# Kernel tuning notes

Hardware: AMD Instinct MI355X
Metric: run time of the kernel (lower is better)

Reference implementation:

```python
import jax, jax.numpy as jnp
import numpy as np

N_QUBITS = 12
N_LAYERS = 6
BATCH = 8192
D_IN = 512


def _apply_1q(state, gate, wire):
    # state: [B] + [2]*n (real), gate: [2,2]. new[j] = sum_i gate[j,i]*old[i]
    s = jnp.moveaxis(state, 1 + wire, -1)
    s = jnp.einsum('...i,ji->...j', s, gate)
    return jnp.moveaxis(s, -1, 1 + wire)


def _apply_cnot(state, ctrl, tgt):
    # flip target amplitude pair where control bit == 1
    s = jnp.moveaxis(state, (1 + ctrl, 1 + tgt), (-2, -1))
    s = jnp.concatenate([s[..., :1, :], s[..., 1:, ::-1]], axis=-2)
    return jnp.moveaxis(s, (-2, -1), (1 + ctrl, 1 + tgt))


def _simulate(angles, weights):
    # angles: [B, n] per-sample RY angles; weights: [L, n] shared RY angles.
    # Circuit: H + RY(angle) per wire on |0>, then L x (RY layer + CNOT chain).
    # All gates are real -> real float32 statevector.
    B, n = angles.shape
    L = weights.shape[0]
    inv_sqrt2 = jnp.float32(1.0 / np.sqrt(2.0))
    half = 0.5 * angles
    c, s = jnp.cos(half), jnp.sin(half)
    # per-wire single-qubit state RY(a) @ H @ |0> = inv_sqrt2 * [c-s, c+s]
    v = inv_sqrt2 * jnp.stack([c - s, c + s], axis=-1)  # [B, n, 2]
    state = v[:, 0]  # [B, 2]
    for w in range(1, n):
        state = jnp.einsum('b...,bj->b...j', state, v[:, w])  # product state
    # state: [B] + [2]*n
    for layer in range(L):
        h = 0.5 * weights[layer]
        cl, sl = jnp.cos(h), jnp.sin(h)
        for w in range(n):
            gate = jnp.stack([jnp.stack([cl[w], -sl[w]]),
                              jnp.stack([sl[w], cl[w]])])
            state = _apply_1q(state, gate, w)
        for w in range(n - 1):
            state = _apply_cnot(state, w, w + 1)
    probs = state * state
    zs = []
    for w in range(n):
        axes = tuple(a for a in range(1, n + 1) if a != 1 + w)
        p = probs.sum(axis=axes)  # [B, 2]
        zs.append(p[:, 0] - p[:, 1])
    return jnp.stack(zs, axis=-1)  # [B, n] = <Z_i>


def setup_inputs() -> dict:
    key = jax.random.key(0)
    ks = jax.random.split(key, 6)
    x = jax.random.normal(ks[0], (BATCH, D_IN), jnp.float32)
    pre_w = jax.random.normal(ks[1], (N_QUBITS, D_IN), jnp.float32) / np.sqrt(D_IN)
    pre_b = jax.random.normal(ks[2], (N_QUBITS,), jnp.float32) * 0.01
    weights = jax.random.normal(ks[3], (N_LAYERS, N_QUBITS), jnp.float32)
    post_w = jax.random.normal(ks[4], (1, N_QUBITS), jnp.float32) / np.sqrt(N_QUBITS)
    post_b = jax.random.normal(ks[5], (1,), jnp.float32) * 0.01
    return {"x": x, "pre_w": pre_w, "pre_b": pre_b, "weights": weights,
            "post_w": post_w, "post_b": post_b}


def reference(x, pre_w, pre_b, weights, post_w, post_b):
    pre = x @ pre_w.T + pre_b                # [B, n_qubits]
    angles = pre * jnp.float32(np.pi / 2.0)  # RY(inputs[i]*pi/2)
    q_out = _simulate(angles, weights)       # [B, n_qubits]
    return q_out @ post_w.T + post_b         # [B, 1]
```

## Files before the change

### kernel.cpp

```cpp
#include <hip/hip_runtime.h>
#include <math.h>

#define NQ 12
#define NL 6
#define BATCHN 8192
#define DIN 512

typedef _Float16 f16;
typedef __attribute__((ext_vector_type(8)))  _Float16 f16x8;
typedef __attribute__((ext_vector_type(16))) float    f32x16;
typedef unsigned int u32;
typedef __attribute__((ext_vector_type(4))) u32 u32x4;
typedef __attribute__((ext_vector_type(2))) int i32x2;


__device__ __forceinline__ u32 pkrtz(float a, float b) {
  auto p = __builtin_amdgcn_cvt_pkrtz(a, b);
  return __builtin_bit_cast(u32, p);
}
__device__ __forceinline__ u32 bperm(int addr, u32 v) {
  return (u32)__builtin_amdgcn_ds_bpermute(addr, (int)v);
}
__device__ __forceinline__ float dppx1(float v) {
  return __int_as_float(__builtin_amdgcn_mov_dpp(__float_as_int(v), 0xB1, 0xF, 0xF, true));
}
__device__ __forceinline__ u32 dppx1u(u32 v) {
  return (u32)__builtin_amdgcn_mov_dpp((int)v, 0xB1, 0xF, 0xF, true);
}
__device__ __forceinline__ float dppx2(float v) {
  return __int_as_float(__builtin_amdgcn_mov_dpp(__float_as_int(v), 0x4E, 0xF, 0xF, true));
}
__device__ __forceinline__ float dppx8(float v) {
  return __int_as_float(__builtin_amdgcn_mov_dpp(__float_as_int(v), 0x128, 0xF, 0xF, true));
}
template <int PAT>
__device__ __forceinline__ float swzf(float v) {
  return __int_as_float(__builtin_amdgcn_ds_swizzle(__float_as_int(v), PAT));
}

#if __has_builtin(__builtin_amdgcn_permlane32_swap)
__device__ __forceinline__ void pswap(u32& a, u32& b) {
  i32x2 r = __builtin_amdgcn_permlane32_swap((int)a, (int)b, false, false);
  a = (u32)r.x; b = (u32)r.y;
}
#else
#define PSWAP_FALLBACK 1
__device__ __forceinline__ void pswap_fb(u32& a, u32& b, bool hi, int axor) {
  u32 xa = bperm(axor, a), xb = bperm(axor, b);
  u32 na = hi ? xb : a;
  u32 nb = hi ? b : xa;
  a = na; b = nb;
}
#endif

__device__ __forceinline__ float wave_sum(float v) {
  v += dppx1(v);
  v += dppx2(v);
  v += swzf<0x101F>(v);
  v += dppx8(v);
  v += swzf<0x401F>(v);
#ifndef PSWAP_FALLBACK
  u32 a = __builtin_bit_cast(u32, v), b = a;
  pswap(a, b);
  return __builtin_bit_cast(float, a) + __builtin_bit_cast(float, b);
#else
  return v + __shfl_xor(v, 32, 64);
#endif
}
__device__ __forceinline__ f16x8 asf(const u32 a[4]) {
  u32x4 v; v.x = a[0]; v.y = a[1]; v.z = a[2]; v.w = a[3];
  return __builtin_bit_cast(f16x8, v);
}
__device__ __forceinline__ f16x8 ldB(const u32* __restrict__ p, int off) {
  u32x4 v = *(const u32x4*)(p + off);
  return __builtin_bit_cast(f16x8, v);
}

__device__ __forceinline__ void sincos_rev(float rev, float* s, float* c) {
  float r = rev - floorf(rev);
#if __has_builtin(__builtin_amdgcn_sinf) && __has_builtin(__builtin_amdgcn_cosf)
  *s = __builtin_amdgcn_sinf(r);
  *c = __builtin_amdgcn_cosf(r);
#else
  const float TWO_PI = 6.28318530717958647693f;
  sincosf(r * TWO_PI, s, c);
#endif
}

__device__ __forceinline__ u32 foldw(u32 w, u32 m) {
  u32 partner = dppx1u(w);
  return (m & partner) | (~m & w);
}

__global__ void setup_mats(const float* __restrict__ weights, u32* __restrict__ Bbuf) {
  const int mm = blockIdx.x >> 3;
  const int l  = mm >> 1;
  const int qs = mm & 1;
  __shared__ float c6[6], s6[6];
  if (threadIdx.x < 6) {
    float h = 0.5f * weights[l * NQ + qs * 6 + threadIdx.x];
    c6[threadIdx.x] = cosf(h);
    s6[threadIdx.x] = sinf(h);
  }
  __syncthreads();
  const int t = (blockIdx.x & 7) * 256 + threadIdx.x;
  const int lane = (t >> 2) & 63;
  const int fk   = t >> 8;
  const int kt   = fk & 3;
  const int nt   = fk >> 2;
  const int n     = nt * 32 + (lane & 31);
  const int kbase = kt * 16 + (lane >> 5) * 8 + (t & 3) * 2;
  float v[2];
  #pragma unroll
  for (int u = 0; u < 2; ++u) {
    int k = kbase + u;
    int bb = k;
    if (l >= 1) { bb ^= bb << 1; bb ^= bb << 2; bb ^= bb << 4; bb &= 63; }
    float prod = 1.f;
    #pragma unroll
    for (int w = 0; w < 6; ++w) {
      const int aw = (n >> w) & 1, bw = (bb >> w) & 1;
      prod *= (aw == bw) ? c6[w] : (aw ? s6[w] : -s6[w]);
    }
    v[u] = prod;
  }
  Bbuf[mm * 2048 + t] = pkrtz(v[0], v[1]);
}

template <bool FOLD>
__device__ __forceinline__ void mm_step(f32x16 (&d)[2][2],
                                        const u32* __restrict__ Bl,
                                        u32 maskA, u32 maskB) {
  f16x8 Bc0 = ldB(Bl, 0 * 256);
  f16x8 Bc1 = ldB(Bl, 4 * 256);
  u32 fr[2][4][4];
  #pragma unroll
  for (int kt = 0; kt < 4; ++kt) {
    const int s  = kt >> 1;
    const int b0 = 4 * ((2 * kt) & 3);
    const int b1 = 4 * ((2 * kt + 1) & 3);
    #pragma unroll
    for (int mt = 0; mt < 2; ++mt) {
      u32 p0a = pkrtz(d[s][mt][b0 + 0], d[s][mt][b0 + 1]);
      u32 p0b = pkrtz(d[s][mt][b0 + 2], d[s][mt][b0 + 3]);
      u32 p1a = pkrtz(d[s][mt][b1 + 0], d[s][mt][b1 + 1]);
      u32 p1b = pkrtz(d[s][mt][b1 + 2], d[s][mt][b1 + 3]);
      if (FOLD) {
        const int PAR4[4] = {0, 1, 1, 0};
        const int ka = (PAR4[b0 >> 2] + s) & 1;
        const int kc = (PAR4[b1 >> 2] + s) & 1;
        p0a = foldw(p0a, ka ? maskB : maskA);
        p0b = foldw(p0b, ka ? maskA : maskB);
        p1a = foldw(p1a, kc ? maskB : maskA);
        p1b = foldw(p1b, kc ? maskA : maskB);
      }
#ifdef PSWAP_FALLBACK
      pswap_fb(p0a, p1a, false, 0);
      pswap_fb(p0b, p1b, false, 0);
#else
      pswap(p0a, p1a);
      pswap(p0b, p1b);
#endif
      fr[mt][kt][0] = p0a;
      fr[mt][kt][1] = p0b;
      fr[mt][kt][2] = p1a;
      fr[mt][kt][3] = p1b;
    }
  }
  #pragma unroll
  for (int kt = 0; kt < 4; ++kt) {
    f16x8 B0 = Bc0, B1 = Bc1;
    if (kt < 3) {
      Bc0 = ldB(Bl, (kt + 1) * 256);
      Bc1 = ldB(Bl, (4 + kt + 1) * 256);
    }
    f16x8 A0 = asf(fr[0][kt]);
    f16x8 A1 = asf(fr[1][kt]);
    if (kt == 0) {
      f32x16 z{};
      d[0][0] = __builtin_amdgcn_mfma_f32_32x32x16_f16(A0, B0, z, 0, 0, 0);
      d[0][1] = __builtin_amdgcn_mfma_f32_32x32x16_f16(A0, B1, z, 0, 0, 0);
      d[1][0] = __builtin_amdgcn_mfma_f32_32x32x16_f16(A1, B0, z, 0, 0, 0);
      d[1][1] = __builtin_amdgcn_mfma_f32_32x32x16_f16(A1, B1, z, 0, 0, 0);
    } else {
      d[0][0] = __builtin_amdgcn_mfma_f32_32x32x16_f16(A0, B0, d[0][0], 0, 0, 0);
      d[0][1] = __builtin_amdgcn_mfma_f32_32x32x16_f16(A0, B1, d[0][1], 0, 0, 0);
      d[1][0] = __builtin_amdgcn_mfma_f32_32x32x16_f16(A1, B0, d[1][0], 0, 0, 0);
      d[1][1] = __builtin_amdgcn_mfma_f32_32x32x16_f16(A1, B1, d[1][1], 0, 0, 0);
    }
  }
}

__global__ void __launch_bounds__(256) __attribute__((amdgpu_waves_per_eu(4, 8)))
dqc_main(const float* __restrict__ x,
         const float* __restrict__ pre_w,
         const float* __restrict__ pre_b,
         const float* __restrict__ weights,
         const float* __restrict__ post_w,
         const float* __restrict__ post_b,
         const u32* __restrict__ Bbuf,
         float* __restrict__ out)
{
  const int lane = threadIdx.x & 63;
  const bool hi  = lane >= 32;
  const int b    = blockIdx.x * 4 + (threadIdx.x >> 6);
  const u32 maskA = hi ? 0x0000FFFFu : 0xFFFF0000u;
  const u32 maskB = ~maskA;

  float acc[NQ];
  const float* xr = x + (size_t)b * DIN + lane * 8;
  const float4 xa = *(const float4*)(xr);
  const float4 xb = *(const float4*)(xr + 4);
  #pragma unroll
  for (int w = 0; w < NQ; ++w) {
    const float* wr = pre_w + w * DIN + lane * 8;
    const float4 wa = *(const float4*)(wr);
    const float4 wb = *(const float4*)(wr + 4);
    acc[w] = xa.x * wa.x + xa.y * wa.y + xa.z * wa.z + xa.w * wa.w
           + xb.x * wb.x + xb.y * wb.y + xb.z * wb.z + xb.w * wb.w;
  }
  #pragma unroll
  for (int w = 0; w < NQ; ++w) acc[w] = wave_sum(acc[w]);

  const float INV_4PI = 0.07957747154594766788f;
  float u0[NQ], u1[NQ];
  #pragma unroll
  for (int w = 0; w < NQ; ++w) {
    const float cw2 = 0.125f + pre_b[w] * 0.125f + weights[w] * INV_4PI;
    const float rev = fmaf(acc[w], 0.125f, cw2);
    sincos_rev(rev, &u1[w], &u0[w]);
  }

  float base8[8];
  #pragma unroll
  for (int j = 0; j < 8; ++j)
    base8[j] = ((j & 1) ? u1[0] : u0[0]) * ((j & 2) ? u1[1] : u0[1]) * ((j & 4) ? u1[2] : u0[2]);
  float hiP[4];
  #pragma unroll
  for (int kt = 0; kt < 4; ++kt)
    hiP[kt] = (hi ? u1[3] : u0[3]) * ((kt & 1) ? u1[4] : u0[4]) * ((kt & 2) ? u1[5] : u0[5]);
  const float q5 = ((lane & 2) ? u1[7] : u0[7]) * ((lane & 4) ? u1[8] : u0[8])
                 * ((lane & 8) ? u1[9] : u0[9]) * ((lane & 16) ? u1[10] : u0[10]);
  const float qA = q5 * ((lane & 1) ? u1[6] : u0[6]);
  const float qB = q5 * ((lane & 1) ? u0[6] : u1[6]);
  const float qeven = hi ? qB : qA;
  const float qodd  = hi ? qA : qB;
  const float qe0 = qeven * u0[11], qo0 = qodd * u0[11];
  const float qe1 = qeven * u1[11], qo1 = qodd * u1[11];

  const u32* BlBase = Bbuf + lane * 4;

  f32x16 d[2][2];
  {
    const u32* Bl2 = BlBase + 2 * 2048;
    f16x8 Ic0 = ldB(Bl2, 0 * 256);
    f16x8 Ic1 = ldB(Bl2, 4 * 256);
    const int PKT[4] = {0, 1, 1, 0};
    const int PDW[4] = {0, 1, 1, 0};
    #pragma unroll
    for (int kt = 0; kt < 4; ++kt) {
      u32 a0[4], a1[4];
      #pragma unroll
      for (int dw = 0; dw < 4; ++dw) {
        const float e0 = base8[2 * dw] * hiP[kt];
        const float e1 = base8[2 * dw + 1] * hiP[kt];
        const bool cls = (PKT[kt] ^ PDW[dw]) != 0;
        a0[dw] = pkrtz((cls ? qo0 : qe0) * e0, (cls ? qe0 : qo0) * e1);
        a1[dw] = pkrtz((cls ? qo1 : qe1) * e0, (cls ? qe1 : qo1) * e1);
      }
      f16x8 B0 = Ic0, B1 = Ic1;
      if (kt < 3) {
        Ic0 = ldB(Bl2, (kt + 1) * 256);
        Ic1 = ldB(Bl2, (4 + kt + 1) * 256);
      }
      f16x8 A0 = asf(a0), A1 = asf(a1);
      if (kt == 0) {
        f32x16 z{};
        d[0][0] = __builtin_amdgcn_mfma_f32_32x32x16_f16(A0, B0, z, 0, 0, 0);
        d[0][1] = __builtin_amdgcn_mfma_f32_32x32x16_f16(A0, B1, z, 0, 0, 0);
        d[1][0] = __builtin_amdgcn_mfma_f32_32x32x16_f16(A1, B0, z, 0, 0, 0);
        d[1][1] = __builtin_amdgcn_mfma_f32_32x32x16_f16(A1, B1, z, 0, 0, 0);
      } else {
        d[0][0] = __builtin_amdgcn_mfma_f32_32x32x16_f16(A0, B0, d[0][0], 0, 0, 0);
        d[0][1] = __builtin_amdgcn_mfma_f32_32x32x16_f16(A0, B1, d[0][1], 0, 0, 0);
        d[1][0] = __builtin_amdgcn_mfma_f32_32x32x16_f16(A1, B0, d[1][0], 0, 0, 0);
        d[1][1] = __builtin_amdgcn_mfma_f32_32x32x16_f16(A1, B1, d[1][1], 0, 0, 0);
      }
    }
  }

  #pragma unroll
  for (int i = 0; i < 4; ++i) {
    mm_step<false>(d, BlBase + (2 * i + 3) * 2048, maskA, maskB);
    mm_step<true >(d, BlBase + (2 * i + 4) * 2048, maskA, maskB);
  }
  mm_step<false>(d, BlBase + 11 * 2048, maskA, maskB);

  const float pw0 = post_w[0], pw1 = post_w[1], pw2 = post_w[2],
              pw3 = post_w[3], pw4 = post_w[4], pw5 = post_w[5];
  float A0s = 0.f, A1s = 0.f, s00 = 0.f, s01 = 0.f, accA = 0.f, accB = 0.f;
  #pragma unroll
  for (int mt = 0; mt < 2; ++mt)
    #pragma unroll
    for (int nt = 0; nt < 2; ++nt)
      #pragma unroll
      for (int r = 0; r < 16; ++r) {
        float v = d[mt][nt][r];
        float sq = v * v;
        const int par0 = (__builtin_popcount(r & 3) + __builtin_popcount(r >> 2) + mt) & 1;
        if (par0) A1s += sq; else A0s += sq;
        if (nt == 0) { if (par0) s01 += sq; else s00 += sq; }
        const int c0 = r & 1;
        const int c1 = (r ^ (r >> 1)) & 1;
        const int c3 = c1 ^ ((r >> 2) & 1);
        const int c4 = c3 ^ ((r >> 3) & 1);
        const int c5 = c4 ^ mt;
        const float ca = (c0 ? -pw0 : pw0) + (c1 ? -pw1 : pw1);
        const float cb = (c1 ? -pw2 : pw2) + (c3 ? -pw3 : pw3)
                       + (c4 ? -pw4 : pw4) + (c5 ? -pw5 : pw5);
        accA = fmaf(ca, sq, accA);
        accB = fmaf(cb, sq, accB);
      }
  const float sgnhi = hi ? -1.f : 1.f;
  const float tot   = A0s + A1s;
  const float diff  = sgnhi * (A0s - A1s);
  const float diffs = sgnhi * (2.f * (s00 - s01) - (A0s - A1s));
  float Sq = 0.f;
  #pragma unroll
  for (int j = 0; j < 5; ++j) {
    const int par = __builtin_popcount(lane & ((2 << j) - 1)) & 1;
    Sq += par ? -post_w[6 + j] : post_w[6 + j];
  }
  const float s5 = (__builtin_popcount(lane & 31) & 1) ? -post_w[11] : post_w[11];
  const float zcomb = accA + sgnhi * accB + diff * Sq + diffs * s5;

  const float tots = wave_sum(tot);
  const float zs   = wave_sum(zcomb);

  if (lane == 0) {
    out[b] = fmaf(zs, 1.0f / tots, post_b[0]);
  }
}

extern "C" void kernel_launch(void* const* d_in, const int* in_sizes, int n_in,
                              void* d_out, int out_size, void* d_ws, size_t ws_size,
                              hipStream_t stream) {
  (void)in_sizes; (void)n_in; (void)out_size; (void)ws_size;
  const float* x       = (const float*)d_in[0];
  const float* pre_w   = (const float*)d_in[1];
  const float* pre_b   = (const float*)d_in[2];
  const float* weights = (const float*)d_in[3];
  const float* post_w  = (const float*)d_in[4];
  const float* post_b  = (const float*)d_in[5];
  float* out = (float*)d_out;
  u32* Bbuf = (u32*)d_ws;

  setup_mats<<<96, 256, 0, stream>>>(weights, Bbuf);
  dqc_main<<<BATCHN / 4, 256, 0, stream>>>(x, pre_w, pre_b, weights,
                                           post_w, post_b, Bbuf, out);
}
```

Before: 117.0 us.

## Stage per-step gate matrices into double-buffered LDS via async global loads

```diff
diff --git a/kernel.cpp b/kernel.cpp
--- a/kernel.cpp
+++ b/kernel.cpp
@@ -76,6 +76,32 @@
   return __builtin_bit_cast(f16x8, v);
 }
 
+#if __has_builtin(__builtin_amdgcn_global_load_lds)
+#define HAVE_GLLDS 1
+__device__ __forceinline__ void stage_mat(const u32* __restrict__ Bg,
+                                          u32* lbuf, int wid, int lane) {
+  #pragma unroll
+  for (int c2 = 0; c2 < 2; ++c2) {
+    const int c = wid * 2 + c2;
+    const u32* g = Bg + c * 256 + lane * 4;
+    u32* l = lbuf + c * 256;
+    __builtin_amdgcn_global_load_lds(
+        (const __attribute__((address_space(1))) u32*)g,
+        (__attribute__((address_space(3))) u32*)l, 16, 0, 0);
+  }
+}
+#else
+__device__ __forceinline__ void stage_mat(const u32* __restrict__ Bg,
+                                          u32* lbuf, int wid, int lane) {
+  #pragma unroll
+  for (int c2 = 0; c2 < 2; ++c2) {
+    const int c = wid * 2 + c2;
+    u32x4 v = *(const u32x4*)(Bg + c * 256 + lane * 4);
+    *(u32x4*)(lbuf + c * 256 + lane * 4) = v;
+  }
+}
+#endif
+
 __device__ __forceinline__ void sincos_rev(float rev, float* s, float* c) {
   float r = rev - floorf(rev);
 #if __has_builtin(__builtin_amdgcn_sinf) && __has_builtin(__builtin_amdgcn_cosf)
@@ -129,7 +155,7 @@
 
 template <bool FOLD>
 __device__ __forceinline__ void mm_step(f32x16 (&d)[2][2],
-                                        const u32* __restrict__ Bl,
+                                        const u32* Bl,
                                         u32 maskA, u32 maskB) {
   f16x8 Bc0 = ldB(Bl, 0 * 256);
   f16x8 Bc1 = ldB(Bl, 4 * 256);
@@ -191,7 +217,7 @@
   }
 }
 
-__global__ void __launch_bounds__(256) __attribute__((amdgpu_waves_per_eu(4, 8)))
+__global__ void __launch_bounds__(256) __attribute__((amdgpu_waves_per_eu(3, 4)))
 dqc_main(const float* __restrict__ x,
          const float* __restrict__ pre_w,
          const float* __restrict__ pre_b,
@@ -202,10 +228,15 @@
          float* __restrict__ out)
 {
   const int lane = threadIdx.x & 63;
+  const int wid  = threadIdx.x >> 6;
   const bool hi  = lane >= 32;
-  const int b    = blockIdx.x * 4 + (threadIdx.x >> 6);
+  const int b    = blockIdx.x * 4 + wid;
   const u32 maskA = hi ? 0x0000FFFFu : 0xFFFF0000u;
   const u32 maskB = ~maskA;
+
+  __shared__ __align__(16) u32 Bs[2][2048];
+  stage_mat(Bbuf + 2 * 2048, &Bs[0][0], wid, lane);
+  stage_mat(Bbuf + 3 * 2048, &Bs[1][0], wid, lane);
 
   float acc[NQ];
   const float* xr = x + (size_t)b * DIN + lane * 8;
@@ -248,13 +279,16 @@
   const float qe0 = qeven * u0[11], qo0 = qodd * u0[11];
   const float qe1 = qeven * u1[11], qo1 = qodd * u1[11];
 
-  const u32* BlBase = Bbuf + lane * 4;
+  asm volatile("s_waitcnt vmcnt(0)" ::: "memory");
+  __syncthreads();
+
+  const u32* B0p = &Bs[0][0] + lane * 4;
+  const u32* B1p = &Bs[1][0] + lane * 4;
 
   f32x16 d[2][2];
   {
-    const u32* Bl2 = BlBase + 2 * 2048;
-    f16x8 Ic0 = ldB(Bl2, 0 * 256);
-    f16x8 Ic1 = ldB(Bl2, 4 * 256);
+    f16x8 Ic0 = ldB(B0p, 0 * 256);
+    f16x8 Ic1 = ldB(B0p, 4 * 256);
     const int PKT[4] = {0, 1, 1, 0};
     const int PDW[4] = {0, 1, 1, 0};
     #pragma unroll
@@ -270,8 +304,8 @@
       }
       f16x8 B0 = Ic0, B1 = Ic1;
       if (kt < 3) {
-        Ic0 = ldB(Bl2, (kt + 1) * 256);
-        Ic1 = ldB(Bl2, (4 + kt + 1) * 256);
+        Ic0 = ldB(B0p, (kt + 1) * 256);
+        Ic1 = ldB(B0p, (4 + kt + 1) * 256);
       }
       f16x8 A0 = asf(a0), A1 = asf(a1);
       if (kt == 0) {
@@ -289,12 +323,33 @@
     }
   }
 
-  #pragma unroll
-  for (int i = 0; i < 4; ++i) {
-    mm_step<false>(d, BlBase + (2 * i + 3) * 2048, maskA, maskB);
-    mm_step<true >(d, BlBase + (2 * i + 4) * 2048, maskA, maskB);
-  }
-  mm_step<false>(d, BlBase + 11 * 2048, maskA, maskB);
+  #define STEP_TAIL(nextmm, bufidx)                                  \
+    do {                                                             \
+      asm volatile("s_waitcnt vmcnt(0)" ::: "memory");               \
+      __syncthreads();                                               \
+      stage_mat(Bbuf + (nextmm) * 2048, &Bs[bufidx][0], wid, lane);  \
+    } while (0)
+
+  STEP_TAIL(4, 0);
+  mm_step<false>(d, B1p, maskA, maskB);
+  STEP_TAIL(5, 1);
+  mm_step<true >(d, B0p, maskA, maskB);
+  STEP_TAIL(6, 0);
+  mm_step<false>(d, B1p, maskA, maskB);
+  STEP_TAIL(7, 1);
+  mm_step<true >(d, B0p, maskA, maskB);
+  STEP_TAIL(8, 0);
+  mm_step<false>(d, B1p, maskA, maskB);
+  STEP_TAIL(9, 1);
+  mm_step<true >(d, B0p, maskA, maskB);
+  STEP_TAIL(10, 0);
+  mm_step<false>(d, B1p, maskA, maskB);
+  STEP_TAIL(11, 1);
+  mm_step<true >(d, B0p, maskA, maskB);
+  asm volatile("s_waitcnt vmcnt(0)" ::: "memory");
+  __syncthreads();
+  mm_step<false>(d, B1p, maskA, maskB);
+  #undef STEP_TAIL
 
   const float pw0 = post_w[0], pw1 = post_w[1], pw2 = post_w[2],
               pw3 = post_w[3], pw4 = post_w[4], pw5 = post_w[5];
```

New measurement: 116.1 us. About the same (-0.8%).
